# Optimization experiments

Hardware: AMD Instinct MI355X
Metric: run time of the kernel (lower is better)

The kernel has to match this reference:

```python
import jax, jax.numpy as jnp
import numpy as np
import math

C, H, L, V = 1024, 16, 2, 32000
D = C // H  # head_dim = 64
FF = 4 * C
B, T = 1, 2048
EPS = 1e-5

def _alibi_slopes(n_heads):
    start = 2 ** (-2 ** (-(math.log2(n_heads) - 3)))
    return np.array([start * start ** i for i in range(n_heads)], dtype=np.float32)

SLOPES = jnp.asarray(_alibi_slopes(H))

def _sym_ln(x, w, b):
    # per-head-channel LayerNorm over head_dim, scalar scale/bias per head
    xh = x.reshape(x.shape[0], x.shape[1], H, D)
    mu = xh.mean(-1, keepdims=True)
    var = ((xh - mu) ** 2).mean(-1, keepdims=True)
    n = (xh - mu) / jnp.sqrt(var + EPS)
    n = n * w[None, None, :, None] + b[None, None, :, None]
    return n.reshape(x.shape)

def _alibi_bias(t):
    pos = jnp.arange(t)[None, :] - jnp.arange(t)[:, None]  # j - i
    pos = jnp.minimum(pos, 0).astype(jnp.float32)
    return SLOPES[:, None, None] * pos[None, :, :]  # (H, T, T)

def _block(x, ln1_w, ln1_b, ln2_w, ln2_b, attn_w, attn_b, v_tmp, proj_tmp, fc_w, fc_b, pw, pb):
    b_, t_, _ = x.shape
    h_in = _sym_ln(x, ln1_w, ln1_b)
    qk = h_in @ attn_w.T + attn_b  # (B, T, 2C)
    q, k = jnp.split(qk, 2, axis=-1)
    # Kronecker/block-diagonal V: per-head (head_dim x head_dim) matmul, x @ M^T per head
    xh = h_in.reshape(b_, t_, H, D)
    v = jnp.einsum('bthd,hed->bthe', xh, v_tmp)  # (B, T, H, D)
    q = q.reshape(b_, t_, H, D).transpose(0, 2, 1, 3)
    k = k.reshape(b_, t_, H, D).transpose(0, 2, 1, 3)
    v = v.transpose(0, 2, 1, 3)
    scale = 1.0 / math.sqrt(D)
    scores = jnp.einsum('bhqd,bhkd->bhqk', q, k) * scale
    scores = scores + _alibi_bias(t_)[None]  # note: no causal mask in original code
    att = jax.nn.softmax(scores, axis=-1)
    y = jnp.einsum('bhqk,bhkd->bhqd', att, v)
    y = y.transpose(0, 2, 1, 3)  # (B, T, H, D)
    y = jnp.einsum('bthd,hed->bthe', y, proj_tmp).reshape(b_, t_, C)
    x = x + y
    h2 = _sym_ln(x, ln2_w, ln2_b)
    f = jax.nn.gelu(h2 @ fc_w.T + fc_b, approximate=False)
    x = x + (f @ pw.T + pb)
    return x

def setup_inputs() -> dict:
    key = jax.random.key(0)
    ks = jax.random.split(key, 12)
    s = 0.02
    return {
        'idx': jax.random.randint(ks[0], (B, T), 0, V, dtype=jnp.int32),
        'wte': jax.random.normal(ks[1], (V, C), jnp.float32) * s,
        'ln1_w': jnp.ones((L, H), jnp.float32),
        'ln1_b': jnp.zeros((L, H), jnp.float32),
        'ln2_w': jnp.ones((L, H), jnp.float32),
        'ln2_b': jnp.zeros((L, H), jnp.float32),
        'lnf_w': jnp.ones((H,), jnp.float32),
        'lnf_b': jnp.zeros((H,), jnp.float32),
        'attn_w': jax.random.normal(ks[2], (L, 2 * C, C), jnp.float32) * s,
        'attn_b': jnp.zeros((L, 2 * C), jnp.float32),
        'v_tmp': jax.random.normal(ks[3], (L, H, D, D), jnp.float32) * s,
        'proj_tmp': jax.random.normal(ks[4], (L, H, D, D), jnp.float32) * s,
        'fc_w': jax.random.normal(ks[5], (L, FF, C), jnp.float32) * s,
        'fc_b': jnp.zeros((L, FF), jnp.float32),
        'proj_w': jax.random.normal(ks[6], (L, C, FF), jnp.float32) * s,
        'proj_b': jnp.zeros((L, C), jnp.float32),
    }

def reference(idx, wte, ln1_w, ln1_b, ln2_w, ln2_b, lnf_w, lnf_b,
              attn_w, attn_b, v_tmp, proj_tmp, fc_w, fc_b, proj_w, proj_b):
    x = wte[idx]  # (B, T, C)
    for l in range(L):
        x = _block(x, ln1_w[l], ln1_b[l], ln2_w[l], ln2_b[l],
                   attn_w[l], attn_b[l], v_tmp[l], proj_tmp[l],
                   fc_w[l], fc_b[l], proj_w[l], proj_b[l])
    x = _sym_ln(x, lnf_w, lnf_b)
    logits = x @ wte.T  # tied lm_head
    return logits
```

## Files before the change

### kernel.cpp

```cpp
#include <hip/hip_runtime.h>
#include <cstdint>
#include <cstddef>

#define T_SEQ 2048
#define C_DIM 1024
#define H_HEADS 16
#define D_HEAD 64
#define FF_DIM 4096
#define V_VOCAB 32000
#define L_LAYERS 2

typedef unsigned short u16;
typedef short bf16x8 __attribute__((ext_vector_type(8)));
typedef float f32x4 __attribute__((ext_vector_type(4)));

__device__ inline u16 f2bf(float f) {
  unsigned u = __float_as_uint(f);
  u += 0x7fffu + ((u >> 16) & 1u);
  return (u16)(u >> 16);
}
__device__ inline float bf2f(u16 h) { return __uint_as_float(((unsigned)h) << 16); }

#define OFF_WTEBF   0ULL
#define OFF_ATTNBF  65536000ULL
#define OFF_FCBF    73924608ULL
#define OFF_PRJBF   90701824ULL
#define OFF_X       107479040ULL
#define OFF_HBF     115867648ULL
#define OFF_QKBF    120061952ULL
#define OFF_VT      128450560ULL
#define OFF_Y       132644864ULL
#define OFF_FBF     141033472ULL
#define OFF_VWBF    157810688ULL
#define OFF_PWBF    158072832ULL
#define ARENA_BYTES 158334976ULL

__device__ __align__(1024) unsigned char g_arena[ARENA_BYTES];

__global__ void cvt_bf16_k(const float4* __restrict__ in, ushort4* __restrict__ out, int n4) {
  int i = blockIdx.x * 256 + threadIdx.x;
  if (i < n4) {
    float4 v = in[i];
    out[i] = make_ushort4(f2bf(v.x), f2bf(v.y), f2bf(v.z), f2bf(v.w));
  }
}

__global__ void cvt_multi_k(const float4* __restrict__ s0, const float4* __restrict__ s1,
                            const float4* __restrict__ s2, const float4* __restrict__ s3,
                            const float4* __restrict__ s4,
                            ushort4* __restrict__ d0, ushort4* __restrict__ d1,
                            ushort4* __restrict__ d2, ushort4* __restrict__ d3,
                            ushort4* __restrict__ d4) {
  int g = blockIdx.x * 256 + threadIdx.x;
  const float4* s; ushort4* d; int off;
  if (g < 1048576)      { s = s0; d = d0; off = g; }
  else if (g < 3145728) { s = s1; d = d1; off = g - 1048576; }
  else if (g < 5242880) { s = s2; d = d2; off = g - 3145728; }
  else if (g < 5275648) { s = s3; d = d3; off = g - 5242880; }
  else                  { s = s4; d = d4; off = g - 5275648; }
  float4 v = s[off];
  d[off] = make_ushort4(f2bf(v.x), f2bf(v.y), f2bf(v.z), f2bf(v.w));
}

__global__ void embed_k(const int* __restrict__ idx, const float4* __restrict__ wte,
                        float4* __restrict__ x) {
  int t = blockIdx.x;
  int r = idx[t];
  x[(size_t)t * 256 + threadIdx.x] = wte[(size_t)r * 256 + threadIdx.x];
}

__global__ void symln_k(const float* __restrict__ x, const float* __restrict__ w,
                        const float* __restrict__ b, u16* __restrict__ out) {
  int t = blockIdx.x;
  int wv = threadIdx.x >> 6, lane = threadIdx.x & 63;
  #pragma unroll
  for (int hh = 0; hh < 4; hh++) {
    int h = wv * 4 + hh;
    float v = x[(size_t)t * C_DIM + h * 64 + lane];
    float s = v, s2 = v * v;
    #pragma unroll
    for (int m = 32; m; m >>= 1) { s += __shfl_xor(s, m); s2 += __shfl_xor(s2, m); }
    float mu = s * (1.f / 64.f);
    float var = s2 * (1.f / 64.f) - mu * mu;
    float n = (v - mu) * rsqrtf(var + 1e-5f) * w[h] + b[h];
    out[(size_t)t * C_DIM + h * 64 + lane] = f2bf(n);
  }
}

template <int NROWS, int ROWBYTES, int WAVES>
__device__ inline void stage_rows(u16* lds, const u16* __restrict__ g, int ld,
                                  int wid, int lane) {
  constexpr int PASSES = (NROWS * ROWBYTES) / (WAVES * 1024);
  #pragma unroll
  for (int i = 0; i < PASSES; i++) {
    int base = (i * WAVES + wid) * 1024;
    int o = base + lane * 16;
    int u = o ^ (((o / ROWBYTES) & 7) << 4);
    int row = u / ROWBYTES, colb = u % ROWBYTES;
    const u16* src = g + (size_t)row * ld + (colb >> 1);
    __builtin_amdgcn_global_load_lds((const __attribute__((address_space(1))) void*)src,
                                     (__attribute__((address_space(3))) void*)(lds + base / 2),
                                     16, 0, 0);
  }
}

__global__ __launch_bounds__(256) void flash_k(const u16* __restrict__ qk,
                                               const u16* __restrict__ vt,
                                               u16* __restrict__ y) {
  int h = blockIdx.y;
  int q0 = blockIdx.x * 64;
  int tid = threadIdx.x, wid = tid >> 6, lane = tid & 63;
  int g4 = lane >> 4, l15 = lane & 15;
  __shared__ u16 Kl[128 * 64];
  __shared__ u16 Vl[64 * 128];
  __shared__ u16 Pl[64 * 128];
  float slope = exp2f(-0.5f * (float)(h + 1));

  bf16x8 qf[2];
  const u16* qb = qk + (size_t)(q0 + wid * 16) * 2048 + h * 64;
  #pragma unroll
  for (int kk = 0; kk < 2; kk++)
    qf[kk] = *(const bf16x8*)(qb + (size_t)l15 * 2048 + kk * 32 + g4 * 8);

  f32x4 lsum = (f32x4){0.f, 0.f, 0.f, 0.f};
  f32x4 oacc[4];
  #pragma unroll
  for (int n = 0; n < 4; n++) oacc[n] = (f32x4){0.f, 0.f, 0.f, 0.f};

  const u16* kbase = qk + 1024 + h * 64;
  const u16* vbase = vt + (size_t)h * 64 * T_SEQ;

  for (int kt = 0; kt < T_SEQ / 128; kt++) {
    int k0 = kt * 128;
    stage_rows<128, 128, 4>(Kl, kbase + (size_t)k0 * 2048, 2048, wid, lane);
    stage_rows<64, 256, 4>(Vl, vbase + k0, T_SEQ, wid, lane);
    __syncthreads();

    f32x4 s[8];
    #pragma unroll
    for (int n = 0; n < 8; n++) s[n] = (f32x4){0.f, 0.f, 0.f, 0.f};
    #pragma unroll
    for (int kk = 0; kk < 2; kk++) {
      #pragma unroll
      for (int n = 0; n < 8; n++) {
        int r = n * 16 + l15;
        int b = (r * 128 + kk * 64 + g4 * 16) ^ ((r & 7) << 4);
        bf16x8 kf = *(const bf16x8*)((const char*)Kl + b);
        s[n] = __builtin_amdgcn_mfma_f32_16x16x32_bf16(qf[kk], kf, s[n], 0, 0, 0);
      }
    }

    int iq = q0 + wid * 16 + g4 * 4;
    #pragma unroll
    for (int n = 0; n < 8; n++) {
      int j = k0 + n * 16 + l15;
      #pragma unroll
      for (int i = 0; i < 4; i++) {
        float v = s[n][i] * 0.125f + slope * fminf((float)(j - (iq + i)), 0.f);
        float p = __expf(v - 8.f);
        lsum[i] += p;
        int pr = wid * 16 + g4 * 4 + i;
        int b = (pr * 256 + (n * 16 + l15) * 2) ^ ((pr & 7) << 4);
        *(u16*)((char*)Pl + b) = f2bf(p);
      }
    }

    #pragma unroll
    for (int kk = 0; kk < 4; kk++) {
      int pr = wid * 16 + l15;
      int pb = (pr * 256 + kk * 64 + g4 * 16) ^ ((pr & 7) << 4);
      bf16x8 pa = *(const bf16x8*)((const char*)Pl + pb);
      #pragma unroll
      for (int n = 0; n < 4; n++) {
        int d = n * 16 + l15;
        int vb = (d * 256 + kk * 64 + g4 * 16) ^ ((d & 7) << 4);
        bf16x8 vf = *(const bf16x8*)((const char*)Vl + vb);
        oacc[n] = __builtin_amdgcn_mfma_f32_16x16x32_bf16(pa, vf, oacc[n], 0, 0, 0);
      }
    }
    __syncthreads();
  }

  #pragma unroll
  for (int i = 0; i < 4; i++) {
    float v = lsum[i];
    #pragma unroll
    for (int msk = 1; msk <= 8; msk <<= 1) v += __shfl_xor(v, msk);
    lsum[i] = v;
  }
  u16* yb = y + (size_t)(q0 + wid * 16) * C_DIM + h * 64;
  #pragma unroll
  for (int n = 0; n < 4; n++)
    #pragma unroll
    for (int i = 0; i < 4; i++)
      yb[(size_t)(g4 * 4 + i) * C_DIM + n * 16 + l15] = f2bf(oacc[n][i] / lsum[i]);
}

#define ASM_VMCNT0 asm volatile("s_waitcnt vmcnt(0)" ::: "memory")

__global__ __launch_bounds__(512, 1) void gemm256_k(const u16* __restrict__ A, int lda,
                                                    const u16* __restrict__ B, int ldb,
                                                    float* __restrict__ C, int ldc,
                                                    int K, int MT) {
  extern __shared__ u16 sm[];
  u16* lsA = sm;
  u16* lsB = sm + 32768;
  int tid = threadIdx.x, wid = tid >> 6, lane = tid & 63;
  int g4 = lane >> 4, l15 = lane & 15;
  int wm = wid >> 2, wn = wid & 3;
  int nwg = gridDim.x, lin = blockIdx.x;
  int chunk = nwg >> 3;
  int w = (lin & 7) * chunk + (lin >> 3);
  int by = w % MT, bx = w / MT;
  const u16* Ab = A + (size_t)(by * 256) * lda;
  const u16* Bb = B + (size_t)(bx * 256) * ldb;

  f32x4 acc[8][4];
  #pragma unroll
  for (int m = 0; m < 8; m++)
    #pragma unroll
    for (int n = 0; n < 4; n++) acc[m][n] = (f32x4){0.f, 0.f, 0.f, 0.f};

  int NT = K >> 6;
  stage_rows<256, 128, 8>(lsA, Ab, lda, wid, lane);
  stage_rows<256, 128, 8>(lsB, Bb, ldb, wid, lane);

  for (int t = 0; t < NT; ++t) {
    int cur = t & 1;
    const char* cA = (const char*)(lsA + cur * 16384);
    const char* cB = (const char*)(lsB + cur * 16384);
    ASM_VMCNT0;
    __builtin_amdgcn_s_barrier();
    __builtin_amdgcn_sched_barrier(0);
    if (t + 1 < NT) {
      stage_rows<256, 128, 8>(lsA + (cur ^ 1) * 16384, Ab + (t + 1) * 64, lda, wid, lane);
      stage_rows<256, 128, 8>(lsB + (cur ^ 1) * 16384, Bb + (t + 1) * 64, ldb, wid, lane);
    }
    #pragma unroll
    for (int kk = 0; kk < 2; kk++) {
      bf16x8 bfr[4], af[8];
      #pragma unroll
      for (int n = 0; n < 4; n++) {
        int r = wn * 64 + n * 16 + l15;
        bfr[n] = *(const bf16x8*)(cB + ((r * 128 + kk * 64 + g4 * 16) ^ ((r & 7) << 4)));
      }
      #pragma unroll
      for (int m = 0; m < 8; m++) {
        int r = wm * 128 + m * 16 + l15;
        af[m] = *(const bf16x8*)(cA + ((r * 128 + kk * 64 + g4 * 16) ^ ((r & 7) << 4)));
      }
      __builtin_amdgcn_s_setprio(1);
      #pragma unroll
      for (int m = 0; m < 8; m++)
        #pragma unroll
        for (int n = 0; n < 4; n++)
          acc[m][n] = __builtin_amdgcn_mfma_f32_16x16x32_bf16(af[m], bfr[n], acc[m][n], 0, 0, 0);
      __builtin_amdgcn_s_setprio(0);
    }
  }

  int gr0 = by * 256 + wm * 128, gc0 = bx * 256 + wn * 64;
  #pragma unroll
  for (int m = 0; m < 8; m++)
    #pragma unroll
    for (int n = 0; n < 4; n++)
      #pragma unroll
      for (int i = 0; i < 4; i++)
        C[(size_t)(gr0 + m * 16 + g4 * 4 + i) * ldc + gc0 + n * 16 + l15] = acc[m][n][i];
}

template <int BM, int BN, int WM, int WN, int EPI, int MT, int GRID>
__global__ void gemm_nt(const u16* __restrict__ A, int lda, long long sA,
                        const u16* __restrict__ B, int ldb, long long sB,
                        void* __restrict__ C, int ldc, long long sC,
                        int K, const float* __restrict__ bias,
                        const float* __restrict__ resid, int ldr) {
  constexpr int RM = BM / WM, RN = BN / WN;
  constexpr int MR = RM / 16, NR = RN / 16;
  __shared__ u16 lsA[BM * 64];
  __shared__ u16 lsB[BN * 64];
  int tid = threadIdx.x, wid = tid >> 6, lane = tid & 63;
  int wm = wid / WN, wn = wid % WN;
  int lin, z;
  if constexpr (GRID == 1) {
    lin = blockIdx.x; z = blockIdx.y;
  } else {
    int nwg = gridDim.x, l0 = blockIdx.x;
    int chunk = nwg >> 3;
    lin = (l0 & 7) * chunk + (l0 >> 3);
    z = 0;
  }
  int by = lin % MT, bx = lin / MT;
  int row0 = by * BM, col0 = bx * BN;
  const u16* Ab = A + (size_t)z * sA + (size_t)row0 * lda;
  const u16* Bb = B + (size_t)z * sB + (size_t)col0 * ldb;
  size_t cz = (size_t)z * sC;

  f32x4 acc[MR][NR];
  #pragma unroll
  for (int m = 0; m < MR; m++)
    #pragma unroll
    for (int n = 0; n < NR; n++) acc[m][n] = (f32x4){0.f, 0.f, 0.f, 0.f};

  for (int k0 = 0; k0 < K; k0 += 64) {
    stage_rows<BM, 128, 4>(lsA, Ab + k0, lda, wid, lane);
    stage_rows<BN, 128, 4>(lsB, Bb + k0, ldb, wid, lane);
    __syncthreads();
    #pragma unroll
    for (int kk = 0; kk < 2; kk++) {
      bf16x8 af[MR], bfr[NR];
      #pragma unroll
      for (int m = 0; m < MR; m++) {
        int r = wm * RM + m * 16 + (lane & 15);
        int bofs = (r * 128 + kk * 64 + ((lane >> 4) * 16)) ^ ((r & 7) << 4);
        af[m] = *(const bf16x8*)((const char*)lsA + bofs);
      }
      #pragma unroll
      for (int n = 0; n < NR; n++) {
        int r = wn * RN + n * 16 + (lane & 15);
        int bofs = (r * 128 + kk * 64 + ((lane >> 4) * 16)) ^ ((r & 7) << 4);
        bfr[n] = *(const bf16x8*)((const char*)lsB + bofs);
      }
      #pragma unroll
      for (int m = 0; m < MR; m++)
        #pragma unroll
        for (int n = 0; n < NR; n++)
          acc[m][n] = __builtin_amdgcn_mfma_f32_16x16x32_bf16(af[m], bfr[n], acc[m][n], 0, 0, 0);
    }
    __syncthreads();
  }

  int rbase = row0 + wm * RM, cbase = col0 + wn * RN;
  #pragma unroll
  for (int m = 0; m < MR; m++)
    #pragma unroll
    for (int n = 0; n < NR; n++)
      #pragma unroll
      for (int i = 0; i < 4; i++) {
        int gr = rbase + m * 16 + ((lane >> 4) * 4) + i;
        int gc = cbase + n * 16 + (lane & 15);
        size_t idx = cz + (size_t)gr * ldc + gc;
        float v = acc[m][n][i];
        if constexpr (EPI == 0) {
          ((float*)C)[idx] = v;
        } else if constexpr (EPI == 1) {
          v += bias[gc];
          ((u16*)C)[idx] = f2bf(v);
        } else if constexpr (EPI == 2) {
          ((u16*)C)[idx] = f2bf(v);
        } else if constexpr (EPI == 3) {
          v += bias[gc];
          v = 0.5f * v * (1.f + erff(v * 0.70710678118654752f));
          ((u16*)C)[idx] = f2bf(v);
        } else if constexpr (EPI == 4) {
          v += bias[gc] + resid[(size_t)gr * ldr + gc];
          ((float*)C)[idx] = v;
        } else {
          ((float*)C)[idx] += v;
        }
      }
}

extern "C" void kernel_launch(void* const* d_in, const int* in_sizes, int n_in,
                              void* d_out, int out_size, void* d_ws, size_t ws_size,
                              hipStream_t stream) {
  (void)in_sizes; (void)n_in; (void)out_size; (void)d_ws; (void)ws_size;
  const int*   idx    = (const int*)d_in[0];
  const float* wte    = (const float*)d_in[1];
  const float* ln1w   = (const float*)d_in[2];
  const float* ln1b   = (const float*)d_in[3];
  const float* ln2w   = (const float*)d_in[4];
  const float* ln2b   = (const float*)d_in[5];
  const float* lnfw   = (const float*)d_in[6];
  const float* lnfb   = (const float*)d_in[7];
  const float* attw   = (const float*)d_in[8];
  const float* attb   = (const float*)d_in[9];
  const float* vtmp   = (const float*)d_in[10];
  const float* ptmp   = (const float*)d_in[11];
  const float* fcw    = (const float*)d_in[12];
  const float* fcb    = (const float*)d_in[13];
  const float* prjw   = (const float*)d_in[14];
  const float* prjb   = (const float*)d_in[15];
  float* out = (float*)d_out;

  unsigned char* ar = nullptr;
  hipGetSymbolAddress((void**)&ar, HIP_SYMBOL(g_arena));
  u16*   wtebf  = (u16*)(ar + OFF_WTEBF);
  u16*   attnbf = (u16*)(ar + OFF_ATTNBF);
  u16*   fcbf   = (u16*)(ar + OFF_FCBF);
  u16*   prjbf  = (u16*)(ar + OFF_PRJBF);
  float* x      = (float*)(ar + OFF_X);
  u16*   hbf    = (u16*)(ar + OFF_HBF);
  u16*   qkbf   = (u16*)(ar + OFF_QKBF);
  u16*   vt     = (u16*)(ar + OFF_VT);
  u16*   ybf    = (u16*)(ar + OFF_Y);
  u16*   fbf    = (u16*)(ar + OFF_FBF);
  u16*   vwbf   = (u16*)(ar + OFF_VWBF);
  u16*   pwbf   = (u16*)(ar + OFF_PWBF);

  hipFuncSetAttribute((const void*)gemm256_k,
                      hipFuncAttributeMaxDynamicSharedMemorySize, 131072);

  cvt_bf16_k<<<dim3((V_VOCAB * C_DIM / 4) / 256), 256, 0, stream>>>(
      (const float4*)wte, (ushort4*)wtebf, V_VOCAB * C_DIM / 4);
  cvt_multi_k<<<dim3(20736), 256, 0, stream>>>(
      (const float4*)attw, (const float4*)fcw, (const float4*)prjw,
      (const float4*)vtmp, (const float4*)ptmp,
      (ushort4*)attnbf, (ushort4*)fcbf, (ushort4*)prjbf,
      (ushort4*)vwbf, (ushort4*)pwbf);

  embed_k<<<dim3(T_SEQ), 256, 0, stream>>>(idx, (const float4*)wte, (float4*)x);

  for (int l = 0; l < L_LAYERS; l++) {
    symln_k<<<dim3(T_SEQ), 256, 0, stream>>>(x, ln1w + l * H_HEADS, ln1b + l * H_HEADS, hbf);
    gemm_nt<64, 128, 2, 2, 1, 32, 0><<<dim3((2 * C_DIM / 128) * (T_SEQ / 64)), 256, 0, stream>>>(
        hbf, C_DIM, 0, attnbf + (size_t)l * 2 * C_DIM * C_DIM, C_DIM, 0,
        qkbf, 2 * C_DIM, 0, C_DIM, attb + l * 2 * C_DIM, nullptr, 0);
    gemm_nt<64, 128, 2, 2, 2, 1, 1><<<dim3(T_SEQ / 128, H_HEADS), 256, 0, stream>>>(
        vwbf + (size_t)l * H_HEADS * 4096, 64, 4096, hbf, C_DIM, 64,
        vt, T_SEQ, (long long)64 * T_SEQ, 64, nullptr, nullptr, 0);
    flash_k<<<dim3(T_SEQ / 64, H_HEADS), 256, 0, stream>>>(qkbf, vt, ybf);
    gemm_nt<128, 64, 4, 1, 5, 16, 1><<<dim3(T_SEQ / 128, H_HEADS), 256, 0, stream>>>(
        ybf, C_DIM, 64, pwbf + (size_t)l * H_HEADS * 4096, 64, 4096,
        x, C_DIM, 64, 64, nullptr, nullptr, 0);
    symln_k<<<dim3(T_SEQ), 256, 0, stream>>>(x, ln2w + l * H_HEADS, ln2b + l * H_HEADS, hbf);
    gemm_nt<128, 128, 2, 2, 3, 16, 0><<<dim3((FF_DIM / 128) * (T_SEQ / 128)), 256, 0, stream>>>(
        hbf, C_DIM, 0, fcbf + (size_t)l * FF_DIM * C_DIM, C_DIM, 0,
        fbf, FF_DIM, 0, C_DIM, fcb + l * FF_DIM, nullptr, 0);
    gemm_nt<64, 128, 2, 2, 4, 32, 0><<<dim3((C_DIM / 128) * (T_SEQ / 64)), 256, 0, stream>>>(
        fbf, FF_DIM, 0, prjbf + (size_t)l * C_DIM * FF_DIM, FF_DIM, 0,
        x, C_DIM, 0, FF_DIM, prjb + l * C_DIM, x, C_DIM);
  }
  symln_k<<<dim3(T_SEQ), 256, 0, stream>>>(x, lnfw, lnfb, hbf);
  gemm256_k<<<dim3((V_VOCAB / 256) * (T_SEQ / 256)), 512, 131072, stream>>>(
      hbf, C_DIM, wtebf, C_DIM, out, V_VOCAB, C_DIM, T_SEQ / 256);
}
```

Measured before the change: 592.8 us.

## Interleave next-tile global-to-LDS prefetch across MFMA phases in lm_head GEMM

Splits each K-tile of the 256x256 GEMM main loop into four phases (two k-halves times two M-halves) and spreads the global_load_lds prefetch passes for the next tile across those phases, instead of issuing them all at the start. Fragment registers for A are halved (4 instead of 8), which lowers register pressure. The aim is to interleave memory issue with MFMA work so the load and compute pipes overlap better. The cost is an extra s_barrier after every phase, which adds synchronization overhead.

```diff
diff --git a/kernel.cpp b/kernel.cpp
--- a/kernel.cpp
+++ b/kernel.cpp
@@ -102,6 +102,18 @@
                                      (__attribute__((address_space(3))) void*)(lds + base / 2),
                                      16, 0, 0);
   }
+}
+
+__device__ inline void stage_pass(u16* lds, const u16* __restrict__ g, int ld,
+                                  int i, int wid, int lane) {
+  int base = (i * 8 + wid) * 1024;
+  int o = base + lane * 16;
+  int u = o ^ (((o >> 7) & 7) << 4);
+  int row = u >> 7, colb = u & 127;
+  const u16* src = g + (size_t)row * ld + (colb >> 1);
+  __builtin_amdgcn_global_load_lds((const __attribute__((address_space(1))) void*)src,
+                                   (__attribute__((address_space(3))) void*)(lds + base / 2),
+                                   16, 0, 0);
 }
 
 __global__ __launch_bounds__(256) void flash_k(const u16* __restrict__ qk,
@@ -229,33 +241,51 @@
     int cur = t & 1;
     const char* cA = (const char*)(lsA + cur * 16384);
     const char* cB = (const char*)(lsB + cur * 16384);
+    u16* nAl = lsA + (cur ^ 1) * 16384;
+    u16* nBl = lsB + (cur ^ 1) * 16384;
+    const u16* gA = Ab + (t + 1) * 64;
+    const u16* gB = Bb + (t + 1) * 64;
+    bool pf = (t + 1 < NT);
+
     ASM_VMCNT0;
     __builtin_amdgcn_s_barrier();
     __builtin_amdgcn_sched_barrier(0);
-    if (t + 1 < NT) {
-      stage_rows<256, 128, 8>(lsA + (cur ^ 1) * 16384, Ab + (t + 1) * 64, lda, wid, lane);
-      stage_rows<256, 128, 8>(lsB + (cur ^ 1) * 16384, Bb + (t + 1) * 64, ldb, wid, lane);
-    }
-    #pragma unroll
-    for (int kk = 0; kk < 2; kk++) {
-      bf16x8 bfr[4], af[8];
-      #pragma unroll
-      for (int n = 0; n < 4; n++) {
-        int r = wn * 64 + n * 16 + l15;
-        bfr[n] = *(const bf16x8*)(cB + ((r * 128 + kk * 64 + g4 * 16) ^ ((r & 7) << 4)));
-      }
-      #pragma unroll
-      for (int m = 0; m < 8; m++) {
-        int r = wm * 128 + m * 16 + l15;
+
+    bf16x8 bfr[4], af[4];
+    #pragma unroll
+    for (int ph = 0; ph < 4; ++ph) {
+      const int kk = ph >> 1, mh = ph & 1;
+      if (mh == 0) {
+        #pragma unroll
+        for (int n = 0; n < 4; n++) {
+          int r = wn * 64 + n * 16 + l15;
+          bfr[n] = *(const bf16x8*)(cB + ((r * 128 + kk * 64 + g4 * 16) ^ ((r & 7) << 4)));
+        }
+      }
+      #pragma unroll
+      for (int m = 0; m < 4; m++) {
+        int r = wm * 128 + mh * 64 + m * 16 + l15;
         af[m] = *(const bf16x8*)(cA + ((r * 128 + kk * 64 + g4 * 16) ^ ((r & 7) << 4)));
       }
+      if (pf) {
+        if (ph == 0) { stage_pass(nAl, gA, lda, 0, wid, lane);
+                       stage_pass(nAl, gA, lda, 1, wid, lane);
+                       stage_pass(nBl, gB, ldb, 0, wid, lane); }
+        else if (ph == 1) { stage_pass(nAl, gA, lda, 2, wid, lane);
+                            stage_pass(nAl, gA, lda, 3, wid, lane);
+                            stage_pass(nBl, gB, ldb, 1, wid, lane); }
+        else if (ph == 2) { stage_pass(nBl, gB, ldb, 2, wid, lane);
+                            stage_pass(nBl, gB, ldb, 3, wid, lane); }
+      }
       __builtin_amdgcn_s_setprio(1);
       #pragma unroll
-      for (int m = 0; m < 8; m++)
+      for (int m = 0; m < 4; m++)
         #pragma unroll
         for (int n = 0; n < 4; n++)
-          acc[m][n] = __builtin_amdgcn_mfma_f32_16x16x32_bf16(af[m], bfr[n], acc[m][n], 0, 0, 0);
+          acc[mh * 4 + m][n] =
+              __builtin_amdgcn_mfma_f32_16x16x32_bf16(af[m], bfr[n], acc[mh * 4 + m][n], 0, 0, 0);
       __builtin_amdgcn_s_setprio(0);
+      __builtin_amdgcn_s_barrier();
     }
   }
 
```

Result: no change. 600.6 us (+1.3%).

## Replace double-buffered LM-head GEMM pipeline with single-buffer static LDS loop

Applied to the files above, without the earlier changes.

The final vocab-projection GEMM drops its double-buffered dynamic-LDS prefetch pipeline and uses a single 64 KB static LDS tile that is loaded, synced, consumed and synced again on each K step. Launch bounds change from one to four blocks per CU and the s_setprio hints are removed. The intent appears to be higher occupancy so that other resident blocks hide global-load latency instead of explicit prefetching. The cost is that each block no longer overlaps its loads with compute, and with 128 accumulator floats per lane the register limit implied by four 512-thread blocks may force spills.

```diff
diff --git a/kernel.cpp b/kernel.cpp
--- a/kernel.cpp
+++ b/kernel.cpp
@@ -196,15 +196,12 @@
       yb[(size_t)(g4 * 4 + i) * C_DIM + n * 16 + l15] = f2bf(oacc[n][i] / lsum[i]);
 }
 
-#define ASM_VMCNT0 asm volatile("s_waitcnt vmcnt(0)" ::: "memory")
-
-__global__ __launch_bounds__(512, 1) void gemm256_k(const u16* __restrict__ A, int lda,
+__global__ __launch_bounds__(512, 4) void gemm256_k(const u16* __restrict__ A, int lda,
                                                     const u16* __restrict__ B, int ldb,
                                                     float* __restrict__ C, int ldc,
                                                     int K, int MT) {
-  extern __shared__ u16 sm[];
-  u16* lsA = sm;
-  u16* lsB = sm + 32768;
+  __shared__ u16 lsA[256 * 64];
+  __shared__ u16 lsB[256 * 64];
   int tid = threadIdx.x, wid = tid >> 6, lane = tid & 63;
   int g4 = lane >> 4, l15 = lane & 15;
   int wm = wid >> 2, wn = wid & 3;
@@ -221,42 +218,30 @@
     #pragma unroll
     for (int n = 0; n < 4; n++) acc[m][n] = (f32x4){0.f, 0.f, 0.f, 0.f};
 
-  int NT = K >> 6;
-  stage_rows<256, 128, 8>(lsA, Ab, lda, wid, lane);
-  stage_rows<256, 128, 8>(lsB, Bb, ldb, wid, lane);
-
-  for (int t = 0; t < NT; ++t) {
-    int cur = t & 1;
-    const char* cA = (const char*)(lsA + cur * 16384);
-    const char* cB = (const char*)(lsB + cur * 16384);
-    ASM_VMCNT0;
-    __builtin_amdgcn_s_barrier();
-    __builtin_amdgcn_sched_barrier(0);
-    if (t + 1 < NT) {
-      stage_rows<256, 128, 8>(lsA + (cur ^ 1) * 16384, Ab + (t + 1) * 64, lda, wid, lane);
-      stage_rows<256, 128, 8>(lsB + (cur ^ 1) * 16384, Bb + (t + 1) * 64, ldb, wid, lane);
-    }
+  for (int k0 = 0; k0 < K; k0 += 64) {
+    stage_rows<256, 128, 8>(lsA, Ab + k0, lda, wid, lane);
+    stage_rows<256, 128, 8>(lsB, Bb + k0, ldb, wid, lane);
+    __syncthreads();
     #pragma unroll
     for (int kk = 0; kk < 2; kk++) {
       bf16x8 bfr[4], af[8];
       #pragma unroll
       for (int n = 0; n < 4; n++) {
         int r = wn * 64 + n * 16 + l15;
-        bfr[n] = *(const bf16x8*)(cB + ((r * 128 + kk * 64 + g4 * 16) ^ ((r & 7) << 4)));
+        bfr[n] = *(const bf16x8*)((const char*)lsB + ((r * 128 + kk * 64 + g4 * 16) ^ ((r & 7) << 4)));
       }
       #pragma unroll
       for (int m = 0; m < 8; m++) {
         int r = wm * 128 + m * 16 + l15;
-        af[m] = *(const bf16x8*)(cA + ((r * 128 + kk * 64 + g4 * 16) ^ ((r & 7) << 4)));
-      }
-      __builtin_amdgcn_s_setprio(1);
+        af[m] = *(const bf16x8*)((const char*)lsA + ((r * 128 + kk * 64 + g4 * 16) ^ ((r & 7) << 4)));
+      }
       #pragma unroll
       for (int m = 0; m < 8; m++)
         #pragma unroll
         for (int n = 0; n < 4; n++)
           acc[m][n] = __builtin_amdgcn_mfma_f32_16x16x32_bf16(af[m], bfr[n], acc[m][n], 0, 0, 0);
-      __builtin_amdgcn_s_setprio(0);
     }
+    __syncthreads();
   }
 
   int gr0 = by * 256 + wm * 128, gc0 = bx * 256 + wn * 64;
@@ -398,9 +383,6 @@
   u16*   vwbf   = (u16*)(ar + OFF_VWBF);
   u16*   pwbf   = (u16*)(ar + OFF_PWBF);
 
-  hipFuncSetAttribute((const void*)gemm256_k,
-                      hipFuncAttributeMaxDynamicSharedMemorySize, 131072);
-
   cvt_bf16_k<<<dim3((V_VOCAB * C_DIM / 4) / 256), 256, 0, stream>>>(
       (const float4*)wte, (ushort4*)wtebf, V_VOCAB * C_DIM / 4);
   cvt_multi_k<<<dim3(20736), 256, 0, stream>>>(
@@ -432,6 +414,6 @@
         x, C_DIM, 0, FF_DIM, prjb + l * C_DIM, x, C_DIM);
   }
   symln_k<<<dim3(T_SEQ), 256, 0, stream>>>(x, lnfw, lnfb, hbf);
-  gemm256_k<<<dim3((V_VOCAB / 256) * (T_SEQ / 256)), 512, 131072, stream>>>(
+  gemm256_k<<<dim3((V_VOCAB / 256) * (T_SEQ / 256)), 512, 0, stream>>>(
       hbf, C_DIM, wtebf, C_DIM, out, V_VOCAB, C_DIM, T_SEQ / 256);
 }
```

Result: slower. 1.435 ms (+142.2%).
